# Optimization experiments

Hardware: AMD Instinct MI355X
Metric: run time of the kernel (lower is better)

The kernel has to match this reference:

```python
import jax, jax.numpy as jnp
import numpy as np

B, C, D, H, CS = 2, 1024, 512, 8, 64  # batch, bindings, d_binding, heads, chunk_size


def setup_inputs() -> dict:
    key = jax.random.key(0)
    ks = jax.random.split(key, 12)
    d = D // H
    def lin(k, out_f, in_f):
        return jax.random.normal(k, (out_f, in_f), jnp.float32) * (1.0 / np.sqrt(in_f))
    return {
        "x": jax.random.normal(ks[0], (B, C, D), jnp.float32),
        "Wq": lin(ks[1], D, D), "bq": jnp.zeros((D,), jnp.float32),
        "Wk": lin(ks[2], D, D), "bk": jnp.zeros((D,), jnp.float32),
        "Wv": lin(ks[3], D, D), "bv": jnp.zeros((D,), jnp.float32),
        "w1": lin(ks[4], d, 3 * d), "b1": jnp.zeros((d,), jnp.float32),
        "w2": lin(ks[5], 1, d), "b2": jnp.zeros((1,), jnp.float32),
        "Wo": lin(ks[6], D, D), "bo": jnp.zeros((D,), jnp.float32),
    }


def reference(x, Wq, bq, Wk, bk, Wv, bv, w1, b1, w2, b2, Wo, bo):
    Bx, Cx, Dx = x.shape
    d = Dx // H
    def heads(W, b):
        y = jnp.einsum('bcD,eD->bce', x, W) + b
        return y.reshape(Bx, Cx, H, d).transpose(0, 2, 1, 3)  # (B,H,C,d)
    q = heads(Wq, bq)
    k = heads(Wk, bk)
    v = heads(Wv, bv)
    # split first MLP layer weight into q / k / q*k blocks
    w1_q, w1_k, w1_qk = w1[:, :d], w1[:, d:2 * d], w1[:, 2 * d:]
    qp = jnp.einsum('bhcd,ed->bhce', q, w1_q)  # (B,H,C,d)
    kp = jnp.einsum('bhcd,ed->bhce', k, w1_k)  # (B,H,C,d)
    nc = Cx // CS
    q_ch = q.reshape(Bx, H, nc, CS, d).transpose(2, 0, 1, 3, 4)   # (nc,B,H,CS,d)
    qp_ch = qp.reshape(Bx, H, nc, CS, d).transpose(2, 0, 1, 3, 4)
    inv_sqrt_d = jnp.float32(1.0 / np.sqrt(d))

    def step(carry, xs):
        qc, qpc = xs  # (B,H,CS,d) each
        # hidden: (B,H,CS,C,d)
        res = qpc[:, :, :, None, :] + kp[:, :, None, :, :] + b1
        inter = qc[:, :, :, None, :] * k[:, :, None, :, :]
        hid = res + jnp.einsum('bhijd,ed->bhije', inter, w1_qk)
        h = jax.nn.gelu(hid, approximate=False)
        scores = (jnp.einsum('bhije,e->bhij', h, w2[0]) + b2[0]) * inv_sqrt_d
        attn = jax.nn.softmax(scores, axis=-1)  # (B,H,CS,C)
        out = jnp.einsum('bhij,bhjd->bhid', attn, v)  # (B,H,CS,d)
        return carry, out

    _, outs = jax.lax.scan(jax.checkpoint(step), None, (q_ch, qp_ch))  # (nc,B,H,CS,d)
    out = outs.transpose(1, 2, 0, 3, 4).reshape(Bx, H, Cx, d)
    out = out.transpose(0, 2, 1, 3).reshape(Bx, Cx, Dx)
    return jnp.einsum('bcD,eD->bce', out, Wo) + bo
```

## Files before the change

kernel.cpp:

```cpp
#include <hip/hip_runtime.h>
#include <cstdint>

typedef unsigned short u16;
typedef unsigned int u32;
typedef __attribute__((ext_vector_type(8))) short short8;
typedef __attribute__((ext_vector_type(4))) float floatx4;
typedef __attribute__((ext_vector_type(2))) float floatx2;

__device__ __forceinline__ float b2f(u16 u) {
    union { unsigned int i; float f; } c; c.i = ((unsigned int)u) << 16; return c.f;
}
__device__ __forceinline__ u16 f2b(float f) {
    union { float f; unsigned int i; } c; c.f = f;
    unsigned int u = c.i;
    u = u + 0x7FFFu + ((u >> 16) & 1u);
    return (u16)(u >> 16);
}
__device__ __forceinline__ float u2f(u32 u) { union { u32 u; float f; } c; c.u = u; return c.f; }

__global__ __launch_bounds__(256) void gemm_qkv(
    const float* __restrict__ x,
    const float* __restrict__ Wq, const float* __restrict__ Wk, const float* __restrict__ Wv,
    const float* __restrict__ bq, const float* __restrict__ bk, const float* __restrict__ bv,
    float* __restrict__ qout, u16* __restrict__ kout,
    u16* __restrict__ vthi, u16* __restrict__ vtlo)
{
    __shared__ u16 xs[64 * 72];
    __shared__ u16 wsl[64 * 72];
    int tid = threadIdx.x;
    int lane = tid & 63;
    int wv = tid >> 6;
    int lo = lane & 15, hi = lane >> 4;
    int which = blockIdx.y >> 3;
    int m0 = blockIdx.x * 64, n0 = (blockIdx.y & 7) * 64;
    const float* W    = which == 0 ? Wq : (which == 1 ? Wk : Wv);
    const float* bias = which == 0 ? bq : (which == 1 ? bk : bv);

    floatx4 acc[4];
#pragma unroll
    for (int mt = 0; mt < 4; ++mt) acc[mt] = (floatx4){0.f, 0.f, 0.f, 0.f};

    for (int k0 = 0; k0 < 512; k0 += 64) {
        __syncthreads();
#pragma unroll
        for (int i = 0; i < 2; ++i) {
            int v = tid + i * 256;
            int row = v >> 3, c8 = (v & 7) * 8;
            const float* ap = x + (m0 + row) * 512 + k0 + c8;
            const float* wp = W + (n0 + row) * 512 + k0 + c8;
            float4 a0 = *(const float4*)(ap);
            float4 a1 = *(const float4*)(ap + 4);
            float4 w0 = *(const float4*)(wp);
            float4 w1v = *(const float4*)(wp + 4);
            union { u16 u[8]; uint4 q; } ca, cw;
            ca.u[0] = f2b(a0.x); ca.u[1] = f2b(a0.y); ca.u[2] = f2b(a0.z); ca.u[3] = f2b(a0.w);
            ca.u[4] = f2b(a1.x); ca.u[5] = f2b(a1.y); ca.u[6] = f2b(a1.z); ca.u[7] = f2b(a1.w);
            cw.u[0] = f2b(w0.x); cw.u[1] = f2b(w0.y); cw.u[2] = f2b(w0.z); cw.u[3] = f2b(w0.w);
            cw.u[4] = f2b(w1v.x); cw.u[5] = f2b(w1v.y); cw.u[6] = f2b(w1v.z); cw.u[7] = f2b(w1v.w);
            *(uint4*)(xs + row * 72 + c8)  = ca.q;
            *(uint4*)(wsl + row * 72 + c8) = cw.q;
        }
        __syncthreads();
#pragma unroll
        for (int ks = 0; ks < 2; ++ks) {
            short8 bfr = *(const short8*)(wsl + (wv * 16 + lo) * 72 + ks * 32 + hi * 8);
#pragma unroll
            for (int mt = 0; mt < 4; ++mt) {
                short8 afr = *(const short8*)(xs + (mt * 16 + lo) * 72 + ks * 32 + hi * 8);
                acc[mt] = __builtin_amdgcn_mfma_f32_16x16x32_bf16(afr, bfr, acc[mt], 0, 0, 0);
            }
        }
    }

    int n = n0 + wv * 16 + lo;
    float bv2 = bias[n];
    if (which == 2) {
        __syncthreads();
        int nl = wv * 16 + lo;
#pragma unroll
        for (int mt = 0; mt < 4; ++mt)
#pragma unroll
            for (int r = 0; r < 4; ++r) {
                int ml = mt * 16 + hi * 4 + r;
                float y = acc[mt][r] + bv2;
                u16 vh = f2b(y);
                u16 vl = f2b(y - b2f(vh));
                xs[nl * 72 + ml]  = vh;
                wsl[nl * 72 + ml] = vl;
            }
        __syncthreads();
        int row = tid >> 2, seg = (tid & 3) * 16;
        int b = m0 >> 10, c0 = m0 & 1023, h2 = n0 >> 6;
        size_t dst = ((size_t)((b * 8 + h2) * 64 + row)) * 1024 + c0 + seg;
        *(uint4*)(vthi + dst)     = *(uint4*)(xs  + row * 72 + seg);
        *(uint4*)(vthi + dst + 8) = *(uint4*)(xs  + row * 72 + seg + 8);
        *(uint4*)(vtlo + dst)     = *(uint4*)(wsl + row * 72 + seg);
        *(uint4*)(vtlo + dst + 8) = *(uint4*)(wsl + row * 72 + seg + 8);
    } else {
        int h = n >> 6, dd = n & 63;
#pragma unroll
        for (int mt = 0; mt < 4; ++mt)
#pragma unroll
            for (int r = 0; r < 4; ++r) {
                int m = m0 + mt * 16 + hi * 4 + r;
                float y = acc[mt][r] + bv2;
                int b = m >> 10, c = m & 1023;
                int idx = (((b * 8 + h) * 1024) + c) * 64 + dd;
                if (which == 0) qout[idx] = y;
                else            kout[idx] = f2b(y);
            }
    }
}

__global__ __launch_bounds__(256) void gemm_out(
    const float* __restrict__ A, const float* __restrict__ W, const float* __restrict__ bias,
    float* __restrict__ outf)
{
    __shared__ u16 xs[64 * 72];
    __shared__ u16 wsl[64 * 72];
    int tid = threadIdx.x;
    int lane = tid & 63;
    int wv = tid >> 6;
    int lo = lane & 15, hi = lane >> 4;
    int m0 = blockIdx.x * 64, n0 = blockIdx.y * 64;

    floatx4 acc[4];
#pragma unroll
    for (int mt = 0; mt < 4; ++mt) acc[mt] = (floatx4){0.f, 0.f, 0.f, 0.f};

    for (int k0 = 0; k0 < 512; k0 += 64) {
        __syncthreads();
#pragma unroll
        for (int i = 0; i < 2; ++i) {
            int v = tid + i * 256;
            int row = v >> 3, c8 = (v & 7) * 8;
            const float* ap = A + (m0 + row) * 512 + k0 + c8;
            const float* wp = W + (n0 + row) * 512 + k0 + c8;
            float4 a0 = *(const float4*)(ap);
            float4 a1 = *(const float4*)(ap + 4);
            float4 w0 = *(const float4*)(wp);
            float4 w1v = *(const float4*)(wp + 4);
            union { u16 u[8]; uint4 q; } ca, cw;
            ca.u[0] = f2b(a0.x); ca.u[1] = f2b(a0.y); ca.u[2] = f2b(a0.z); ca.u[3] = f2b(a0.w);
            ca.u[4] = f2b(a1.x); ca.u[5] = f2b(a1.y); ca.u[6] = f2b(a1.z); ca.u[7] = f2b(a1.w);
            cw.u[0] = f2b(w0.x); cw.u[1] = f2b(w0.y); cw.u[2] = f2b(w0.z); cw.u[3] = f2b(w0.w);
            cw.u[4] = f2b(w1v.x); cw.u[5] = f2b(w1v.y); cw.u[6] = f2b(w1v.z); cw.u[7] = f2b(w1v.w);
            *(uint4*)(xs + row * 72 + c8)  = ca.q;
            *(uint4*)(wsl + row * 72 + c8) = cw.q;
        }
        __syncthreads();
#pragma unroll
        for (int ks = 0; ks < 2; ++ks) {
            short8 bfr = *(const short8*)(wsl + (wv * 16 + lo) * 72 + ks * 32 + hi * 8);
#pragma unroll
            for (int mt = 0; mt < 4; ++mt) {
                short8 afr = *(const short8*)(xs + (mt * 16 + lo) * 72 + ks * 32 + hi * 8);
                acc[mt] = __builtin_amdgcn_mfma_f32_16x16x32_bf16(afr, bfr, acc[mt], 0, 0, 0);
            }
        }
    }

    int n = n0 + wv * 16 + lo;
    float bv = bias[n];
#pragma unroll
    for (int mt = 0; mt < 4; ++mt)
#pragma unroll
        for (int r = 0; r < 4; ++r) {
            int m = m0 + mt * 16 + hi * 4 + r;
            outf[m * 512 + n] = acc[mt][r] + bv;
        }
}

__global__ __launch_bounds__(256, 4) void attn18(
    const float* __restrict__ qf, const u16* __restrict__ kb,
    const u16* __restrict__ vthi, const u16* __restrict__ vtlo,
    const float* __restrict__ w1, const float* __restrict__ b1, const float* __restrict__ w2,
    float* __restrict__ ao)
{
    __shared__ float q_l[4 * 64];
    __shared__ __align__(16) u16 plds[2 * 4 * 528];
    __shared__ float l_sh[4];
    int tid = threadIdx.x;
    int lane = tid & 63;
    int wv = tid >> 6;
    int lo = lane & 15, hi = lane >> 4;
    int bh = blockIdx.x >> 8;
    int qbase = (blockIdx.x & 255) << 2;
    int qi = qbase | wv;

    const float NA = -2.45546696f;

    for (int i = tid; i < 2112; i += 256) ((u32*)plds)[i] = 0;

    q_l[wv * 64 + lane] = qf[(bh * 1024 + qi) * 64 + lane];

    float qpacc = b1[lane];
#pragma unroll
    for (int d8 = 0; d8 < 64; d8 += 8) {
        float4 wa = *(const float4*)(w1 + lane * 192 + d8);
        float4 wb = *(const float4*)(w1 + lane * 192 + d8 + 4);
        const float* q8 = q_l + wv * 64 + d8;
        qpacc = __builtin_fmaf(q8[0], wa.x, qpacc);
        qpacc = __builtin_fmaf(q8[1], wa.y, qpacc);
        qpacc = __builtin_fmaf(q8[2], wa.z, qpacc);
        qpacc = __builtin_fmaf(q8[3], wa.w, qpacc);
        qpacc = __builtin_fmaf(q8[4], wb.x, qpacc);
        qpacc = __builtin_fmaf(q8[5], wb.y, qpacc);
        qpacc = __builtin_fmaf(q8[6], wb.z, qpacc);
        qpacc = __builtin_fmaf(q8[7], wb.w, qpacc);
    }
    qpacc *= NA;

    u32 wcp[4][2];
    float w2row = w2[lane] * -0.07344288f;
#pragma unroll
    for (int mt = 0; mt < 4; ++mt)
#pragma unroll
        for (int h2 = 0; h2 < 2; ++h2) {
            int e0 = mt * 16 + hi * 4 + h2 * 2;
            u32 lo16 = (u32)f2b(__shfl(w2row, e0));
            u32 hi16 = (u32)f2b(__shfl(w2row, e0 + 1));
            wcp[mt][h2] = (hi16 << 16) | lo16;
        }

    float qv2[2][8];
#pragma unroll
    for (int ks = 0; ks < 2; ++ks)
#pragma unroll
        for (int j = 0; j < 8; ++j)
            qv2[ks][j] = q_l[wv * 64 + ks * 32 + hi * 8 + j];

    short8 af[4][2];
#pragma unroll
    for (int mt = 0; mt < 4; ++mt) {
        const float* wr = w1 + (mt * 16 + lo) * 192;
#pragma unroll
        for (int ks = 0; ks < 2; ++ks) {
            int dd0 = ks * 32 + hi * 8;
            float4 a0 = *(const float4*)(wr + 128 + dd0);
            float4 a1 = *(const float4*)(wr + 128 + dd0 + 4);
            float4 k0 = *(const float4*)(wr + 64 + dd0);
            float4 k1 = *(const float4*)(wr + 64 + dd0 + 4);
            union { u16 u[8]; short8 s; } cv;
            cv.u[0] = f2b(NA * __builtin_fmaf(qv2[ks][0], a0.x, k0.x));
            cv.u[1] = f2b(NA * __builtin_fmaf(qv2[ks][1], a0.y, k0.y));
            cv.u[2] = f2b(NA * __builtin_fmaf(qv2[ks][2], a0.z, k0.z));
            cv.u[3] = f2b(NA * __builtin_fmaf(qv2[ks][3], a0.w, k0.w));
            cv.u[4] = f2b(NA * __builtin_fmaf(qv2[ks][4], a1.x, k1.x));
            cv.u[5] = f2b(NA * __builtin_fmaf(qv2[ks][5], a1.y, k1.y));
            cv.u[6] = f2b(NA * __builtin_fmaf(qv2[ks][6], a1.z, k1.z));
            cv.u[7] = f2b(NA * __builtin_fmaf(qv2[ks][7], a1.w, k1.w));
            af[mt][ks] = cv.s;
        }
    }

    floatx4 qpinit[4];
    {
        const floatx4 z = (floatx4){0.f, 0.f, 0.f, 0.f};
        union { u16 u[8]; short8 s; } bb;
#pragma unroll
        for (int i = 0; i < 8; ++i) bb.u[i] = 0;
        bb.u[0] = (hi == 0) ? (u16)0x3F80 : (u16)0;
#pragma unroll
        for (int mt = 0; mt < 4; ++mt) {
            float qpv = __shfl(qpacc, mt * 16 + lo);
            union { u16 u[8]; short8 s; } aa;
#pragma unroll
            for (int i = 0; i < 8; ++i) aa.u[i] = 0;
            aa.u[0] = (hi == 0) ? f2b(qpv) : (u16)0;
            qpinit[mt] = __builtin_amdgcn_mfma_f32_16x16x32_bf16(aa.s, bb.s, z, 0, 0, 0);
        }
    }

    __syncthreads();

    float l_run = 0.f;
    floatx4 pvacc = (floatx4){0.f, 0.f, 0.f, 0.f};

    const u16* kc = kb + bh * 65536 + lo * 64 + hi * 8;
    const u16* vhp = vthi + bh * 65536 + (wv * 16 + lo) * 1024 + hi * 8;
    const u16* vlp = vtlo + bh * 65536 + (wv * 16 + lo) * 1024 + hi * 8;

    short8 bf[2][2];
    {
        uint4 k00 = *(const uint4*)(kc);
        uint4 k01 = *(const uint4*)(kc + 32);
        uint4 k10 = *(const uint4*)(kc + 1024);
        uint4 k11 = *(const uint4*)(kc + 1056);
        bf[0][0] = *(short8*)&k00; bf[0][1] = *(short8*)&k01;
        bf[1][0] = *(short8*)&k10; bf[1][1] = *(short8*)&k11;
    }

    for (int g = 0; g < 8; ++g) {
        u16* gw = plds + (g & 1) * (4 * 528);
#pragma unroll
        for (int c = 0; c < 4; ++c) {
            floatx2 s0v = (floatx2){0.f, 0.f};
            floatx2 s1v = (floatx2){0.f, 0.f};

            floatx4 aP[2], aN[2];
            aP[0] = __builtin_amdgcn_mfma_f32_16x16x32_bf16(af[0][0], bf[0][0], qpinit[0], 0, 0, 0);
            aP[0] = __builtin_amdgcn_mfma_f32_16x16x32_bf16(af[0][1], bf[0][1], aP[0], 0, 0, 0);
            aP[1] = __builtin_amdgcn_mfma_f32_16x16x32_bf16(af[0][0], bf[1][0], qpinit[0], 0, 0, 0);
            aP[1] = __builtin_amdgcn_mfma_f32_16x16x32_bf16(af[0][1], bf[1][1], aP[1], 0, 0, 0);

#pragma unroll
            for (int mt = 0; mt < 4; ++mt) {
                if (mt < 3) {
                    aN[0] = __builtin_amdgcn_mfma_f32_16x16x32_bf16(af[mt + 1][0], bf[0][0], qpinit[mt + 1], 0, 0, 0);
                    aN[0] = __builtin_amdgcn_mfma_f32_16x16x32_bf16(af[mt + 1][1], bf[0][1], aN[0], 0, 0, 0);
                    aN[1] = __builtin_amdgcn_mfma_f32_16x16x32_bf16(af[mt + 1][0], bf[1][0], qpinit[mt + 1], 0, 0, 0);
                    aN[1] = __builtin_amdgcn_mfma_f32_16x16x32_bf16(af[mt + 1][1], bf[1][1], aN[1], 0, 0, 0);
                } else {
                    kc += 2048;
                    uint4 k00 = *(const uint4*)(kc);
                    uint4 k01 = *(const uint4*)(kc + 32);
                    uint4 k10 = *(const uint4*)(kc + 1024);
                    uint4 k11 = *(const uint4*)(kc + 1056);
                    bf[0][0] = *(short8*)&k00; bf[0][1] = *(short8*)&k01;
                    bf[1][0] = *(short8*)&k10; bf[1][1] = *(short8*)&k11;
                }

#pragma unroll
                for (int h2 = 0; h2 < 2; ++h2) {
                    u32 wp = wcp[mt][h2];
                    floatx2 wv2 = (floatx2){u2f(wp << 16), u2f(wp & 0xFFFF0000u)};
#pragma unroll
                    for (int t = 0; t < 2; ++t) {
                        floatx2 x = (floatx2){aP[t][h2 * 2 + 0], aP[t][h2 * 2 + 1]};
                        floatx2 ex = (floatx2){__builtin_amdgcn_exp2f(x.x),
                                               __builtin_amdgcn_exp2f(x.y)};
                        floatx2 a = ex + 1.0f;
                        float rc = __builtin_amdgcn_rcpf(a.x * a.y);
                        floatx2 sw = (floatx2){a.y, a.x};
                        floatx2 contrib = (x * wv2) * (sw * rc);
                        if (t == 0) s0v += contrib; else s1v += contrib;
                    }
                }
                aP[0] = aN[0];
                aP[1] = aN[1];
            }

            float s0 = s0v.x + s0v.y, s1 = s1v.x + s1v.y;
            s0 += __shfl_xor(s0, 16); s0 += __shfl_xor(s0, 32);
            s1 += __shfl_xor(s1, 16); s1 += __shfl_xor(s1, 32);

            float p0 = __builtin_amdgcn_exp2f(s0 - 16.0f);
            float p1 = __builtin_amdgcn_exp2f(s1 - 16.0f);
            u16 ph0 = f2b(p0);
            u16 ph1 = f2b(p1);
            l_run += b2f(ph0) + b2f(ph1);

            u16* pw = gw + c * 528;
            if (lane < 16) {
                pw[((lo >> 3) * 16 + wv) * 8 + (lo & 7)] = ph0;
                pw[((2 + (lo >> 3)) * 16 + wv) * 8 + (lo & 7)] = ph1;
            }
        }

        __syncthreads();

#pragma unroll
        for (int c = 0; c < 4; ++c) {
            uint4 vh = *(const uint4*)(vhp + c * 32);
            uint4 vl = *(const uint4*)(vlp + c * 32);
            short8 pf = *(const short8*)(gw + c * 528 + lane * 8);
            pvacc = __builtin_amdgcn_mfma_f32_16x16x32_bf16(pf, *(short8*)&vh, pvacc, 0, 0, 0);
            pvacc = __builtin_amdgcn_mfma_f32_16x16x32_bf16(pf, *(short8*)&vl, pvacc, 0, 0, 0);
        }
        vhp += 128;
        vlp += 128;
    }

    float l = l_run;
    l += __shfl_xor(l, 1); l += __shfl_xor(l, 2);
    l += __shfl_xor(l, 4); l += __shfl_xor(l, 8);
    if (lane == 0) l_sh[wv] = l;
    __syncthreads();

    if (hi == 0) {
        int b = bh >> 3, h = bh & 7;
#pragma unroll
        for (int q = 0; q < 4; ++q) {
            float outv = pvacc[q] * __builtin_amdgcn_rcpf(l_sh[q]);
            ao[((b * 1024 + qbase + q) * 512) + h * 64 + wv * 16 + lo] = outv;
        }
    }
}

extern "C" void kernel_launch(void* const* d_in, const int* in_sizes, int n_in,
                              void* d_out, int out_size, void* d_ws, size_t ws_size,
                              hipStream_t stream)
{
    (void)in_sizes; (void)n_in; (void)out_size; (void)ws_size;
    const float* x  = (const float*)d_in[0];
    const float* Wq = (const float*)d_in[1];
    const float* bq = (const float*)d_in[2];
    const float* Wk = (const float*)d_in[3];
    const float* bk = (const float*)d_in[4];
    const float* Wv = (const float*)d_in[5];
    const float* bv = (const float*)d_in[6];
    const float* w1 = (const float*)d_in[7];
    const float* b1 = (const float*)d_in[8];
    const float* w2 = (const float*)d_in[9];
    const float* Wo = (const float*)d_in[11];
    const float* bo = (const float*)d_in[12];

    char* ws = (char*)d_ws;
    float* q_ws = (float*)(ws);
    u16*   k_ws = (u16*)(ws + (4u << 20));
    u16*   vthi = (u16*)(ws + (6u << 20));
    u16*   vtlo = (u16*)(ws + (8u << 20));
    float* a_ws = (float*)(ws + (10u << 20));

    dim3 blk(256);
    hipLaunchKernelGGL(gemm_qkv, dim3(32, 24), blk, 0, stream,
                       x, Wq, Wk, Wv, bq, bk, bv, q_ws, k_ws, vthi, vtlo);
    hipLaunchKernelGGL(attn18, dim3(4096), blk, 0, stream,
                       q_ws, k_ws, vthi, vtlo, w1, b1, w2, a_ws);
    hipLaunchKernelGGL(gemm_out, dim3(32, 8), blk, 0, stream, a_ws, Wo, bo, (float*)d_out);
}
```

Measured before the change: 553.2 us.

## Make attention waves independent with per-wave PV MFMA and retiled V layout

```diff
diff --git a/kernel.cpp b/kernel.cpp
--- a/kernel.cpp
+++ b/kernel.cpp
@@ -91,7 +91,9 @@
         __syncthreads();
         int row = tid >> 2, seg = (tid & 3) * 16;
         int b = m0 >> 10, c0 = m0 & 1023, h2 = n0 >> 6;
-        size_t dst = ((size_t)((b * 8 + h2) * 64 + row)) * 1024 + c0 + seg;
+        int cc = c0 + seg;
+        size_t dst = (size_t)(b * 8 + h2) * 65536 + (cc >> 5) * 2048
+                   + (row >> 4) * 512 + (row & 15) * 32 + (cc & 31);
         *(uint4*)(vthi + dst)     = *(uint4*)(xs  + row * 72 + seg);
         *(uint4*)(vthi + dst + 8) = *(uint4*)(xs  + row * 72 + seg + 8);
         *(uint4*)(vtlo + dst)     = *(uint4*)(wsl + row * 72 + seg);
@@ -171,15 +173,14 @@
         }
 }
 
-__global__ __launch_bounds__(256, 4) void attn18(
+__global__ __launch_bounds__(256, 4) void attn19(
     const float* __restrict__ qf, const u16* __restrict__ kb,
     const u16* __restrict__ vthi, const u16* __restrict__ vtlo,
     const float* __restrict__ w1, const float* __restrict__ b1, const float* __restrict__ w2,
     float* __restrict__ ao)
 {
     __shared__ float q_l[4 * 64];
-    __shared__ __align__(16) u16 plds[2 * 4 * 528];
-    __shared__ float l_sh[4];
+    __shared__ __align__(16) u16 p_sw[4 * 32];
     int tid = threadIdx.x;
     int lane = tid & 63;
     int wv = tid >> 6;
@@ -189,8 +190,6 @@
     int qi = qbase | wv;
 
     const float NA = -2.45546696f;
-
-    for (int i = tid; i < 2112; i += 256) ((u32*)plds)[i] = 0;
 
     q_l[wv * 64 + lane] = qf[(bh * 1024 + qi) * 64 + lane];
 
@@ -212,15 +211,19 @@
     qpacc *= NA;
 
     u32 wcp[4][2];
+    u32 qpp[4][2];
     float w2row = w2[lane] * -0.07344288f;
 #pragma unroll
     for (int mt = 0; mt < 4; ++mt)
 #pragma unroll
         for (int h2 = 0; h2 < 2; ++h2) {
             int e0 = mt * 16 + hi * 4 + h2 * 2;
-            u32 lo16 = (u32)f2b(__shfl(w2row, e0));
-            u32 hi16 = (u32)f2b(__shfl(w2row, e0 + 1));
-            wcp[mt][h2] = (hi16 << 16) | lo16;
+            u32 wlo = (u32)f2b(__shfl(w2row, e0));
+            u32 whi = (u32)f2b(__shfl(w2row, e0 + 1));
+            wcp[mt][h2] = (whi << 16) | wlo;
+            u32 qlo = (u32)f2b(__shfl(qpacc, e0));
+            u32 qhi = (u32)f2b(__shfl(qpacc, e0 + 1));
+            qpp[mt][h2] = (qhi << 16) | qlo;
         }
 
     float qv2[2][8];
@@ -254,32 +257,16 @@
         }
     }
 
-    floatx4 qpinit[4];
-    {
-        const floatx4 z = (floatx4){0.f, 0.f, 0.f, 0.f};
-        union { u16 u[8]; short8 s; } bb;
-#pragma unroll
-        for (int i = 0; i < 8; ++i) bb.u[i] = 0;
-        bb.u[0] = (hi == 0) ? (u16)0x3F80 : (u16)0;
-#pragma unroll
-        for (int mt = 0; mt < 4; ++mt) {
-            float qpv = __shfl(qpacc, mt * 16 + lo);
-            union { u16 u[8]; short8 s; } aa;
-#pragma unroll
-            for (int i = 0; i < 8; ++i) aa.u[i] = 0;
-            aa.u[0] = (hi == 0) ? f2b(qpv) : (u16)0;
-            qpinit[mt] = __builtin_amdgcn_mfma_f32_16x16x32_bf16(aa.s, bb.s, z, 0, 0, 0);
-        }
-    }
-
-    __syncthreads();
-
     float l_run = 0.f;
-    floatx4 pvacc = (floatx4){0.f, 0.f, 0.f, 0.f};
+    floatx4 pv[4];
+#pragma unroll
+    for (int dt = 0; dt < 4; ++dt) pv[dt] = (floatx4){0.f, 0.f, 0.f, 0.f};
+    const floatx4 Z = (floatx4){0.f, 0.f, 0.f, 0.f};
 
     const u16* kc = kb + bh * 65536 + lo * 64 + hi * 8;
-    const u16* vhp = vthi + bh * 65536 + (wv * 16 + lo) * 1024 + hi * 8;
-    const u16* vlp = vtlo + bh * 65536 + (wv * 16 + lo) * 1024 + hi * 8;
+    const u16* vph = vthi + bh * 65536 + lo * 32 + hi * 8;
+    const u16* vpl = vtlo + bh * 65536 + lo * 32 + hi * 8;
+    u16* psw = p_sw + wv * 32;
 
     short8 bf[2][2];
     {
@@ -291,100 +278,106 @@
         bf[1][0] = *(short8*)&k10; bf[1][1] = *(short8*)&k11;
     }
 
-    for (int g = 0; g < 8; ++g) {
-        u16* gw = plds + (g & 1) * (4 * 528);
-#pragma unroll
-        for (int c = 0; c < 4; ++c) {
-            floatx2 s0v = (floatx2){0.f, 0.f};
-            floatx2 s1v = (floatx2){0.f, 0.f};
-
-            floatx4 aP[2], aN[2];
-            aP[0] = __builtin_amdgcn_mfma_f32_16x16x32_bf16(af[0][0], bf[0][0], qpinit[0], 0, 0, 0);
-            aP[0] = __builtin_amdgcn_mfma_f32_16x16x32_bf16(af[0][1], bf[0][1], aP[0], 0, 0, 0);
-            aP[1] = __builtin_amdgcn_mfma_f32_16x16x32_bf16(af[0][0], bf[1][0], qpinit[0], 0, 0, 0);
-            aP[1] = __builtin_amdgcn_mfma_f32_16x16x32_bf16(af[0][1], bf[1][1], aP[1], 0, 0, 0);
-
-#pragma unroll
-            for (int mt = 0; mt < 4; ++mt) {
-                if (mt < 3) {
-                    aN[0] = __builtin_amdgcn_mfma_f32_16x16x32_bf16(af[mt + 1][0], bf[0][0], qpinit[mt + 1], 0, 0, 0);
-                    aN[0] = __builtin_amdgcn_mfma_f32_16x16x32_bf16(af[mt + 1][1], bf[0][1], aN[0], 0, 0, 0);
-                    aN[1] = __builtin_amdgcn_mfma_f32_16x16x32_bf16(af[mt + 1][0], bf[1][0], qpinit[mt + 1], 0, 0, 0);
-                    aN[1] = __builtin_amdgcn_mfma_f32_16x16x32_bf16(af[mt + 1][1], bf[1][1], aN[1], 0, 0, 0);
-                } else {
-                    kc += 2048;
-                    uint4 k00 = *(const uint4*)(kc);
-                    uint4 k01 = *(const uint4*)(kc + 32);
-                    uint4 k10 = *(const uint4*)(kc + 1024);
-                    uint4 k11 = *(const uint4*)(kc + 1056);
-                    bf[0][0] = *(short8*)&k00; bf[0][1] = *(short8*)&k01;
-                    bf[1][0] = *(short8*)&k10; bf[1][1] = *(short8*)&k11;
+    for (int jc = 0; jc < 32; ++jc) {
+        uint4 vh0 = *(const uint4*)(vph);
+        uint4 vh1 = *(const uint4*)(vph + 512);
+        uint4 vh2 = *(const uint4*)(vph + 1024);
+        uint4 vh3 = *(const uint4*)(vph + 1536);
+
+        floatx2 s0v = (floatx2){0.f, 0.f};
+        floatx2 s1v = (floatx2){0.f, 0.f};
+
+        floatx4 aP[2], aN[2];
+        aP[0] = __builtin_amdgcn_mfma_f32_16x16x32_bf16(af[0][0], bf[0][0], Z, 0, 0, 0);
+        aP[0] = __builtin_amdgcn_mfma_f32_16x16x32_bf16(af[0][1], bf[0][1], aP[0], 0, 0, 0);
+        aP[1] = __builtin_amdgcn_mfma_f32_16x16x32_bf16(af[0][0], bf[1][0], Z, 0, 0, 0);
+        aP[1] = __builtin_amdgcn_mfma_f32_16x16x32_bf16(af[0][1], bf[1][1], aP[1], 0, 0, 0);
+
+#pragma unroll
+        for (int mt = 0; mt < 4; ++mt) {
+            if (mt < 3) {
+                aN[0] = __builtin_amdgcn_mfma_f32_16x16x32_bf16(af[mt + 1][0], bf[0][0], Z, 0, 0, 0);
+                aN[0] = __builtin_amdgcn_mfma_f32_16x16x32_bf16(af[mt + 1][1], bf[0][1], aN[0], 0, 0, 0);
+                aN[1] = __builtin_amdgcn_mfma_f32_16x16x32_bf16(af[mt + 1][0], bf[1][0], Z, 0, 0, 0);
+                aN[1] = __builtin_amdgcn_mfma_f32_16x16x32_bf16(af[mt + 1][1], bf[1][1], aN[1], 0, 0, 0);
+            } else {
+                kc += 2048;
+                uint4 k00 = *(const uint4*)(kc);
+                uint4 k01 = *(const uint4*)(kc + 32);
+                uint4 k10 = *(const uint4*)(kc + 1024);
+                uint4 k11 = *(const uint4*)(kc + 1056);
+                bf[0][0] = *(short8*)&k00; bf[0][1] = *(short8*)&k01;
+                bf[1][0] = *(short8*)&k10; bf[1][1] = *(short8*)&k11;
+            }
+
+#pragma unroll
+            for (int h2 = 0; h2 < 2; ++h2) {
+                u32 wp = wcp[mt][h2];
+                floatx2 wv2 = (floatx2){u2f(wp << 16), u2f(wp & 0xFFFF0000u)};
+                u32 qp = qpp[mt][h2];
+                floatx2 qv = (floatx2){u2f(qp << 16), u2f(qp & 0xFFFF0000u)};
+#pragma unroll
+                for (int t = 0; t < 2; ++t) {
+                    floatx2 x = (floatx2){aP[t][h2 * 2 + 0], aP[t][h2 * 2 + 1]} + qv;
+                    floatx2 ex = (floatx2){__builtin_amdgcn_exp2f(x.x),
+                                           __builtin_amdgcn_exp2f(x.y)};
+                    floatx2 a = ex + 1.0f;
+                    float rc = __builtin_amdgcn_rcpf(a.x * a.y);
+                    floatx2 sw = (floatx2){a.y, a.x};
+                    floatx2 contrib = (x * wv2) * (sw * rc);
+                    if (t == 0) s0v += contrib; else s1v += contrib;
                 }
-
-#pragma unroll
-                for (int h2 = 0; h2 < 2; ++h2) {
-                    u32 wp = wcp[mt][h2];
-                    floatx2 wv2 = (floatx2){u2f(wp << 16), u2f(wp & 0xFFFF0000u)};
-#pragma unroll
-                    for (int t = 0; t < 2; ++t) {
-                        floatx2 x = (floatx2){aP[t][h2 * 2 + 0], aP[t][h2 * 2 + 1]};
-                        floatx2 ex = (floatx2){__builtin_amdgcn_exp2f(x.x),
-                                               __builtin_amdgcn_exp2f(x.y)};
-                        floatx2 a = ex + 1.0f;
-                        float rc = __builtin_amdgcn_rcpf(a.x * a.y);
-                        floatx2 sw = (floatx2){a.y, a.x};
-                        floatx2 contrib = (x * wv2) * (sw * rc);
-                        if (t == 0) s0v += contrib; else s1v += contrib;
-                    }
-                }
-                aP[0] = aN[0];
-                aP[1] = aN[1];
-            }
-
-            float s0 = s0v.x + s0v.y, s1 = s1v.x + s1v.y;
-            s0 += __shfl_xor(s0, 16); s0 += __shfl_xor(s0, 32);
-            s1 += __shfl_xor(s1, 16); s1 += __shfl_xor(s1, 32);
-
-            float p0 = __builtin_amdgcn_exp2f(s0 - 16.0f);
-            float p1 = __builtin_amdgcn_exp2f(s1 - 16.0f);
-            u16 ph0 = f2b(p0);
-            u16 ph1 = f2b(p1);
-            l_run += b2f(ph0) + b2f(ph1);
-
-            u16* pw = gw + c * 528;
-            if (lane < 16) {
-                pw[((lo >> 3) * 16 + wv) * 8 + (lo & 7)] = ph0;
-                pw[((2 + (lo >> 3)) * 16 + wv) * 8 + (lo & 7)] = ph1;
-            }
-        }
-
-        __syncthreads();
-
-#pragma unroll
-        for (int c = 0; c < 4; ++c) {
-            uint4 vh = *(const uint4*)(vhp + c * 32);
-            uint4 vl = *(const uint4*)(vlp + c * 32);
-            short8 pf = *(const short8*)(gw + c * 528 + lane * 8);
-            pvacc = __builtin_amdgcn_mfma_f32_16x16x32_bf16(pf, *(short8*)&vh, pvacc, 0, 0, 0);
-            pvacc = __builtin_amdgcn_mfma_f32_16x16x32_bf16(pf, *(short8*)&vl, pvacc, 0, 0, 0);
-        }
-        vhp += 128;
-        vlp += 128;
+            }
+            aP[0] = aN[0];
+            aP[1] = aN[1];
+        }
+
+        uint4 vl0 = *(const uint4*)(vpl);
+        uint4 vl1 = *(const uint4*)(vpl + 512);
+        uint4 vl2 = *(const uint4*)(vpl + 1024);
+        uint4 vl3 = *(const uint4*)(vpl + 1536);
+
+        float s0 = s0v.x + s0v.y, s1 = s1v.x + s1v.y;
+        s0 += __shfl_xor(s0, 16); s0 += __shfl_xor(s0, 32);
+        s1 += __shfl_xor(s1, 16); s1 += __shfl_xor(s1, 32);
+
+        float p0 = __builtin_amdgcn_exp2f(s0 - 16.0f);
+        float p1 = __builtin_amdgcn_exp2f(s1 - 16.0f);
+        u16 ph0 = f2b(p0);
+        u16 ph1 = f2b(p1);
+        l_run += b2f(ph0) + b2f(ph1);
+
+        if (lane < 16) {
+            psw[lo]      = ph0;
+            psw[16 + lo] = ph1;
+        }
+        short8 pf = *(const short8*)(psw + hi * 8);
+
+        pv[0] = __builtin_amdgcn_mfma_f32_16x16x32_bf16(pf, *(short8*)&vh0, pv[0], 0, 0, 0);
+        pv[1] = __builtin_amdgcn_mfma_f32_16x16x32_bf16(pf, *(short8*)&vh1, pv[1], 0, 0, 0);
+        pv[2] = __builtin_amdgcn_mfma_f32_16x16x32_bf16(pf, *(short8*)&vh2, pv[2], 0, 0, 0);
+        pv[3] = __builtin_amdgcn_mfma_f32_16x16x32_bf16(pf, *(short8*)&vh3, pv[3], 0, 0, 0);
+        pv[0] = __builtin_amdgcn_mfma_f32_16x16x32_bf16(pf, *(short8*)&vl0, pv[0], 0, 0, 0);
+        pv[1] = __builtin_amdgcn_mfma_f32_16x16x32_bf16(pf, *(short8*)&vl1, pv[1], 0, 0, 0);
+        pv[2] = __builtin_amdgcn_mfma_f32_16x16x32_bf16(pf, *(short8*)&vl2, pv[2], 0, 0, 0);
+        pv[3] = __builtin_amdgcn_mfma_f32_16x16x32_bf16(pf, *(short8*)&vl3, pv[3], 0, 0, 0);
+
+        vph += 2048;
+        vpl += 2048;
     }
 
     float l = l_run;
     l += __shfl_xor(l, 1); l += __shfl_xor(l, 2);
     l += __shfl_xor(l, 4); l += __shfl_xor(l, 8);
-    if (lane == 0) l_sh[wv] = l;
-    __syncthreads();
+    float rl = __builtin_amdgcn_rcpf(l);
 
     if (hi == 0) {
         int b = bh >> 3, h = bh & 7;
-#pragma unroll
-        for (int q = 0; q < 4; ++q) {
-            float outv = pvacc[q] * __builtin_amdgcn_rcpf(l_sh[q]);
-            ao[((b * 1024 + qbase + q) * 512) + h * 64 + wv * 16 + lo] = outv;
-        }
+        float* dst = ao + ((size_t)(b * 1024 + qi) * 512) + h * 64 + lo;
+        dst[0]  = pv[0][0] * rl;
+        dst[16] = pv[1][0] * rl;
+        dst[32] = pv[2][0] * rl;
+        dst[48] = pv[3][0] * rl;
     }
 }
 
@@ -416,7 +409,7 @@
     dim3 blk(256);
     hipLaunchKernelGGL(gemm_qkv, dim3(32, 24), blk, 0, stream,
                        x, Wq, Wk, Wv, bq, bk, bv, q_ws, k_ws, vthi, vtlo);
-    hipLaunchKernelGGL(attn18, dim3(4096), blk, 0, stream,
+    hipLaunchKernelGGL(attn19, dim3(4096), blk, 0, stream,
                        q_ws, k_ws, vthi, vtlo, w1, b1, w2, a_ws);
     hipLaunchKernelGGL(gemm_out, dim3(32, 8), blk, 0, stream, a_ws, Wo, bo, (float*)d_out);
 }
```

Result: slower. 865.4 us (+56.4%).
